# Kernel optimization log

Measured on AMD Instinct MI355X. Metric: run time of the kernel, lower is better.

Reference implementation:

```python
import jax, jax.numpy as jnp
import numpy as np

PHI_C = 0.9
ALPHA = 0.9
EPS = 1e-06
K_MAX = 100


def setup_inputs() -> dict:
    key = jax.random.key(0)
    k1, k2, k3 = jax.random.split(key, 3)
    B, D_IN, D_H, D_OUT = 16384, 1024, 4096, 1024
    x = jax.random.normal(k1, (B, D_IN), dtype=jnp.float32)
    W1 = jax.random.normal(k2, (D_IN, D_H), dtype=jnp.float32) * 0.02
    b1 = jnp.zeros((D_H,), dtype=jnp.float32)
    W2 = jax.random.normal(k3, (D_H, D_OUT), dtype=jnp.float32) * 0.02
    b2 = jnp.zeros((D_OUT,), dtype=jnp.float32)
    return {"x": x, "W1": W1, "b1": b1, "W2": W2, "b2": b2}


def _base_net(x, W1, b1, W2, b2):
    h = jax.nn.relu(x @ W1 + b1)
    return h @ W2 + b2  # [B, D_OUT]


def _fixed_point(out):
    # y_{k+1} = y_k + alpha * phi_c * tanh(out - y_k), with early exit when
    # max|y_{k+1} - y_k| < eps (the converging step IS applied, as in torch).
    y0 = jnp.zeros_like(out)

    def step(carry, _):
        y, done = carry
        y_next = y + ALPHA * PHI_C * jnp.tanh(out - y)
        converged = jnp.max(jnp.abs(y_next - y)) < EPS
        y_new = jnp.where(done, y, y_next)
        return (y_new, done | converged), None

    (y, _), _ = jax.lax.scan(step, (y0, jnp.array(False)), None, length=K_MAX)
    return y


def reference(x, W1, b1, W2, b2):
    out = _base_net(x, W1, b1, W2, b2)
    return _fixed_point(out)
```

## Files before the change

kernel.cpp:

```cpp
#include <hip/hip_runtime.h>
#include <hip/hip_bf16.h>
#include <stdint.h>


#define DEV __device__ __forceinline__

typedef short bf16x8 __attribute__((ext_vector_type(8)));
typedef float f32x4 __attribute__((ext_vector_type(4)));

typedef __attribute__((address_space(1))) const unsigned char* gptr1_t;
typedef __attribute__((address_space(3))) unsigned char* lptr3_t;

DEV void async_copy16(const void* g, void* l) {
  __builtin_amdgcn_global_load_lds((gptr1_t)g, (lptr3_t)l, 16, 0, 0);
}

DEV unsigned short f2bf(float f) {
  union { float f; unsigned u; } v; v.f = f;
  unsigned u = v.u + 0x7FFFu + ((v.u >> 16) & 1u);
  return (unsigned short)(u >> 16);
}

#define BAR()  __builtin_amdgcn_s_barrier()
#define VMW(n) asm volatile("s_waitcnt vmcnt(" #n ")" ::: "memory")


__global__ void cvt_f32_bf16(const float4* __restrict__ in,
                             ushort4* __restrict__ out, int n4) {
  int i = blockIdx.x * blockDim.x + threadIdx.x;
  if (i >= n4) return;
  float4 v = in[i];
  ushort4 o;
  o.x = f2bf(v.x); o.y = f2bf(v.y); o.z = f2bf(v.z); o.w = f2bf(v.w);
  out[i] = o;
}

__global__ void transpose_f32_bf16(const float* __restrict__ in,
                                   unsigned short* __restrict__ out,
                                   int R, int C) {
  __shared__ float tile[32][33];
  int c0 = blockIdx.x * 32, r0 = blockIdx.y * 32;
  int tx = threadIdx.x, ty = threadIdx.y;
#pragma unroll
  for (int i = 0; i < 32; i += 8)
    tile[ty + i][tx] = in[(long)(r0 + ty + i) * C + (c0 + tx)];
  __syncthreads();
#pragma unroll
  for (int i = 0; i < 32; i += 8)
    out[(long)(c0 + ty + i) * R + (r0 + tx)] = f2bf(tile[tx][ty + i]);
}


#define LDA(base, m, ks) \
  (*(const bf16x8*)((base) + abase + (m) * 2048 + (c0 ^ ((ks) << 6))))
#define LDB(base, n, ks) \
  (*(const bf16x8*)((base) + bbase + (n) * 2048 + (c0 ^ ((ks) << 6))))

#define RD_A(dst, base, m0_)                                   \
  _Pragma("unroll") for (int m_ = 0; m_ < 4; ++m_) {           \
    dst[m_][0] = LDA(base, (m0_) + m_, 0);                     \
    dst[m_][1] = LDA(base, (m0_) + m_, 1);                     \
  }
#define RD_B(dst, base, n0_)                                   \
  _Pragma("unroll") for (int n_ = 0; n_ < 2; ++n_) {           \
    dst[n_][0] = LDB(base, (n0_) + n_, 0);                     \
    dst[n_][1] = LDB(base, (n0_) + n_, 1);                     \
  }

#define QUAD(MB, NB, AF, BF)                                                \
  do {                                                                      \
    __builtin_amdgcn_s_setprio(1);                                          \
    _Pragma("unroll") for (int m_ = 0; m_ < 4; ++m_)                        \
    _Pragma("unroll") for (int n_ = 0; n_ < 2; ++n_) {                      \
      acc[(MB) + m_][(NB) + n_] = __builtin_amdgcn_mfma_f32_16x16x32_bf16(  \
          AF[m_][0], BF[n_][0], acc[(MB) + m_][(NB) + n_], 0, 0, 0);        \
      acc[(MB) + m_][(NB) + n_] = __builtin_amdgcn_mfma_f32_16x16x32_bf16(  \
          AF[m_][1], BF[n_][1], acc[(MB) + m_][(NB) + n_], 0, 0, 0);        \
    }                                                                       \
    __builtin_amdgcn_s_setprio(0);                                          \
  } while (0)

#define ST_A_LO(dstw, koff) { async_copy16(gA[0] + (koff), (dstw));          \
                              async_copy16(gA[2] + (koff), (dstw) + 16384); }
#define ST_A_HI(dstw, koff) { async_copy16(gA[1] + (koff), (dstw) + 8192);   \
                              async_copy16(gA[3] + (koff), (dstw) + 24576); }
#define ST_B_LO(dstw, koff) { async_copy16(gB[0] + (koff), (dstw));          \
                              async_copy16(gB[1] + (koff), (dstw) + 8192); }
#define ST_B_HI(dstw, koff) { async_copy16(gB[2] + (koff), (dstw) + 16384);  \
                              async_copy16(gB[3] + (koff), (dstw) + 24576); }


__global__ __launch_bounds__(512, 2)
void gemm_w8p(const unsigned short* __restrict__ A,
              const unsigned short* __restrict__ BT,
              const float* __restrict__ bias,
              unsigned short* __restrict__ O,
              int K, int Ndim) {
  extern __shared__ char lds[];
  const char* aE = lds;
  const char* aO = lds + 32768;
  const char* bE = lds + 65536;
  const char* bO = lds + 98304;

  const int tid = threadIdx.x;
  const int wave = tid >> 6, lane = tid & 63;
  const int wr = wave >> 2, wc = wave & 3;

  char* aEw = (char*)aE + wave * 1024;
  char* aOw = (char*)aO + wave * 1024;
  char* bEw = (char*)bE + wave * 1024;
  char* bOw = (char*)bO + wave * 1024;

  const int xcd = blockIdx.x & 7;
  const int jj = blockIdx.x >> 3;
  const int grp = ((xcd >> 1) << 2) | (jj >> 3);
  const int bn = ((xcd & 1) << 3) | (jj & 7);
  const int n0 = bn << 8;
  const int m0base = grp << 10;

  const int srow = tid >> 3;
  const int sk = ((tid & 7) ^ (srow & 7)) << 3;
  const unsigned short* gA[4];
  const unsigned short* gB[4];
#pragma unroll
  for (int c = 0; c < 4; ++c) {
    gA[c] = A + (size_t)(m0base + c * 64 + srow) * K + sk;
    gB[c] = BT + (size_t)(n0 + c * 64 + srow) * K + sk;
  }

  const int lr = lane & 15, lg = lane >> 4;
  const int c0 = ((lg ^ (lr & 7)) << 4);
  const int abase = (wr * 128 + lr) * 128;
  const int bbase = (wc * 64 + lr) * 128;
  const int ccol = n0 + wc * 64;

  f32x4 acc[8][4] = {};
  bf16x8 af[4][2], b01[2][2], b23[2][2];
  float bv[4];
#pragma unroll
  for (int n = 0; n < 4; ++n) bv[n] = bias[ccol + n * 16 + lr];

#define AOFF(g) ((size_t)((g) >> 4) * ((size_t)K << 8) + (size_t)(((g) & 15) << 6))
#define BOFF(g) ((size_t)(((g) & 15) << 6))

#define PEPI(j_)                                                              \
  { const int crow = m0base + (j_) * 256 + wr * 128;                          \
    _Pragma("unroll") for (int m = 0; m < 8; ++m)                             \
    _Pragma("unroll") for (int jq = 0; jq < 4; ++jq) {                        \
      size_t r = (size_t)(crow + m * 16 + lg * 4 + jq) * Ndim;                \
      _Pragma("unroll") for (int n = 0; n < 4; ++n) {                         \
        float v = acc[m][n][jq] + bv[n];                                      \
        O[r + ccol + n * 16 + lr] = f2bf(fmaxf(v, 0.0f));                     \
      } } }

#define ZEROACC()                                                             \
  _Pragma("unroll") for (int m = 0; m < 8; ++m)                               \
  _Pragma("unroll") for (int n = 0; n < 4; ++n)                               \
    acc[m][n] = (f32x4){0.f, 0.f, 0.f, 0.f};

  ST_B_LO(bEw, 0);        ST_B_HI(bEw, 0);
  ST_A_LO(aEw, 0);        ST_A_HI(aEw, 0);
  ST_B_LO(bOw, BOFF(1));  ST_B_HI(bOw, BOFF(1));
  VMW(4);
  BAR();

  for (int it = 0; it < 31; ++it) {
    const int gE = 2 * it, gO = 2 * it + 1;
    RD_B(b01, bE, 0); RD_A(af, aE, 0); RD_B(b23, bE, 2);
    ST_A_LO(aOw, AOFF(gE + 1)); ST_A_HI(aOw, AOFF(gE + 1));
    QUAD(0, 0, af, b01); QUAD(0, 2, af, b23);
    BAR();
    RD_A(af, aE, 4);
    ST_B_LO(bEw, BOFF(gE + 2)); ST_B_HI(bEw, BOFF(gE + 2));
    QUAD(4, 2, af, b23); QUAD(4, 0, af, b01);
    VMW(4); BAR();
    RD_B(b01, bO, 0); RD_A(af, aO, 0); RD_B(b23, bO, 2);
    ST_A_LO(aEw, AOFF(gO + 1)); ST_A_HI(aEw, AOFF(gO + 1));
    QUAD(0, 0, af, b01); QUAD(0, 2, af, b23);
    BAR();
    RD_A(af, aO, 4);
    ST_B_LO(bOw, BOFF(gO + 2)); ST_B_HI(bOw, BOFF(gO + 2));
    QUAD(4, 2, af, b23); QUAD(4, 0, af, b01);
    VMW(4); BAR();
    if ((it & 7) == 7) {
      PEPI(gO >> 4);
      ZEROACC();
    }
  }
  RD_B(b01, bE, 0); RD_A(af, aE, 0); RD_B(b23, bE, 2);
  ST_A_LO(aOw, AOFF(63)); ST_A_HI(aOw, AOFF(63));
  QUAD(0, 0, af, b01); QUAD(0, 2, af, b23);
  BAR();
  RD_A(af, aE, 4);
  QUAD(4, 2, af, b23); QUAD(4, 0, af, b01);
  VMW(0); BAR();
  RD_B(b01, bO, 0); RD_A(af, aO, 0); RD_B(b23, bO, 2);
  QUAD(0, 0, af, b01); QUAD(0, 2, af, b23);
  BAR();
  RD_A(af, aO, 4);
  QUAD(4, 2, af, b23); QUAD(4, 0, af, b01);
  PEPI(3);
#undef PEPI
#undef ZEROACC
#undef AOFF
#undef BOFF
}


template <bool RELU_BF16>
__global__ __launch_bounds__(512, 2)
void gemm_w8(const unsigned short* __restrict__ A,
             const unsigned short* __restrict__ BT,
             const float* __restrict__ bias,
             void* __restrict__ Cout,
             int M, int N, int K, int nbn_shift) {
  extern __shared__ char lds[];
  const char* aE = lds;
  const char* aO = lds + 32768;
  const char* bE = lds + 65536;
  const char* bO = lds + 98304;

  const int tid = threadIdx.x;
  const int wave = tid >> 6, lane = tid & 63;
  const int wr = wave >> 2, wc = wave & 3;

  char* aEw = (char*)aE + wave * 1024;
  char* aOw = (char*)aO + wave * 1024;
  char* bEw = (char*)bE + wave * 1024;
  char* bOw = (char*)bO + wave * 1024;

  const int nwg = gridDim.x;
  const int wg = blockIdx.x;
  const int swz = (wg & 7) * (nwg >> 3) + (wg >> 3);
  const int bm = swz >> nbn_shift;
  const int bn = swz & ((1 << nbn_shift) - 1);
  const int m0 = bm << 8, n0 = bn << 8;

  const int srow = tid >> 3;
  const int sk = ((tid & 7) ^ (srow & 7)) << 3;
  const unsigned short* gA[4];
  const unsigned short* gB[4];
#pragma unroll
  for (int c = 0; c < 4; ++c) {
    gA[c] = A + (size_t)(m0 + c * 64 + srow) * K + sk;
    gB[c] = BT + (size_t)(n0 + c * 64 + srow) * K + sk;
  }

  const int lr = lane & 15, lg = lane >> 4;
  const int c0 = ((lg ^ (lr & 7)) << 4);
  const int abase = (wr * 128 + lr) * 128;
  const int bbase = (wc * 64 + lr) * 128;

  f32x4 acc[8][4] = {};
  bf16x8 af[4][2], b01[2][2], b23[2][2];

  ST_B_LO(bEw, 0);  ST_B_HI(bEw, 0);
  ST_A_LO(aEw, 0);  ST_A_HI(aEw, 0);
  ST_B_LO(bOw, 64); ST_B_HI(bOw, 64);
  VMW(4);
  BAR();

  const int NT = K >> 6;

  for (int it = 0; it < (NT - 2) / 2; ++it) {
    const int kE = (2 * it) << 6;
    RD_B(b01, bE, 0); RD_A(af, aE, 0); RD_B(b23, bE, 2);
    ST_A_LO(aOw, kE + 64); ST_A_HI(aOw, kE + 64);
    QUAD(0, 0, af, b01); QUAD(0, 2, af, b23);
    BAR();
    RD_A(af, aE, 4);
    ST_B_LO(bEw, kE + 128); ST_B_HI(bEw, kE + 128);
    QUAD(4, 2, af, b23); QUAD(4, 0, af, b01);
    VMW(4); BAR();
    RD_B(b01, bO, 0); RD_A(af, aO, 0); RD_B(b23, bO, 2);
    ST_A_LO(aEw, kE + 128); ST_A_HI(aEw, kE + 128);
    QUAD(0, 0, af, b01); QUAD(0, 2, af, b23);
    BAR();
    RD_A(af, aO, 4);
    ST_B_LO(bOw, kE + 192); ST_B_HI(bOw, kE + 192);
    QUAD(4, 2, af, b23); QUAD(4, 0, af, b01);
    VMW(4); BAR();
  }
  {
    const int kL = (NT - 1) << 6;
    RD_B(b01, bE, 0); RD_A(af, aE, 0); RD_B(b23, bE, 2);
    ST_A_LO(aOw, kL); ST_A_HI(aOw, kL);
    QUAD(0, 0, af, b01); QUAD(0, 2, af, b23);
    BAR();
    RD_A(af, aE, 4);
    QUAD(4, 2, af, b23); QUAD(4, 0, af, b01);
    VMW(0); BAR();
    RD_B(b01, bO, 0); RD_A(af, aO, 0); RD_B(b23, bO, 2);
    QUAD(0, 0, af, b01); QUAD(0, 2, af, b23);
    BAR();
    RD_A(af, aO, 4);
    QUAD(4, 2, af, b23); QUAD(4, 0, af, b01);
  }

  const int ccol = n0 + wc * 64;
  const int crow = m0 + wr * 128;
  float bv[4];
#pragma unroll
  for (int n = 0; n < 4; ++n) bv[n] = bias[ccol + n * 16 + lr];

  if (RELU_BF16) {
    unsigned short* O = (unsigned short*)Cout;
#pragma unroll
    for (int m = 0; m < 8; ++m)
#pragma unroll
      for (int j = 0; j < 4; ++j) {
        size_t r = (size_t)(crow + m * 16 + lg * 4 + j) * N;
#pragma unroll
        for (int n = 0; n < 4; ++n) {
          float v = acc[m][n][j] + bv[n];
          O[r + ccol + n * 16 + lr] = f2bf(fmaxf(v, 0.0f));
        }
      }
  } else {
    float* O = (float*)Cout;
#pragma unroll
    for (int m = 0; m < 8; ++m)
#pragma unroll
      for (int j = 0; j < 4; ++j) {
        size_t r = (size_t)(crow + m * 16 + lg * 4 + j) * N;
#pragma unroll
        for (int n = 0; n < 4; ++n)
          O[r + ccol + n * 16 + lr] = acc[m][n][j] + bv[n];
      }
  }
}


extern "C" void kernel_launch(void* const* d_in, const int* in_sizes, int n_in,
                              void* d_out, int out_size, void* d_ws,
                              size_t ws_size, hipStream_t stream) {
  const float* x  = (const float*)d_in[0];
  const float* W1 = (const float*)d_in[1];
  const float* b1 = (const float*)d_in[2];
  const float* W2 = (const float*)d_in[3];
  const float* b2 = (const float*)d_in[4];
  float* out = (float*)d_out;

  const int B = 16384, DIN = 1024, DH = 4096, DOUT = 1024;

  size_t need = (size_t)B * DIN * 2 + (size_t)DIN * DH * 2 +
                (size_t)DH * DOUT * 2 + (size_t)B * DH * 2;
  if (ws_size < need) return;

  char* ws = (char*)d_ws;
  unsigned short* xb  = (unsigned short*)ws;  ws += (size_t)B * DIN * 2;
  unsigned short* w1t = (unsigned short*)ws;  ws += (size_t)DIN * DH * 2;
  unsigned short* w2t = (unsigned short*)ws;  ws += (size_t)DH * DOUT * 2;
  unsigned short* h   = (unsigned short*)ws;

  hipFuncSetAttribute((const void*)gemm_w8p,
                      hipFuncAttributeMaxDynamicSharedMemorySize, 131072);
  hipFuncSetAttribute((const void*)gemm_w8<false>,
                      hipFuncAttributeMaxDynamicSharedMemorySize, 131072);

  int n4 = B * DIN / 4;
  cvt_f32_bf16<<<n4 / 256, 256, 0, stream>>>((const float4*)x, (ushort4*)xb, n4);
  transpose_f32_bf16<<<dim3(DH / 32, DIN / 32), dim3(32, 8), 0, stream>>>(W1, w1t, DIN, DH);
  transpose_f32_bf16<<<dim3(DOUT / 32, DH / 32), dim3(32, 8), 0, stream>>>(W2, w2t, DH, DOUT);

  gemm_w8p<<<dim3(256), 512, 131072, stream>>>(xb, w1t, b1, h, DIN, DH);
  gemm_w8<false><<<dim3((B / 256) * (DOUT / 256)), 512, 131072, stream>>>(
      h, w2t, b2, out, B, DOUT, DH, 2);
}
```

Before: 264.4 us.

## Triple-buffer A tiles in first GEMM and use nontemporal stores for hidden output

The first GEMM's A operand moves from a two-stage to a three-stage LDS ring, with B staying double-buffered, so loads are issued two k-steps ahead. LDS use rises from 128 KiB to 160 KiB and the wait count is relaxed accordingly. The hidden-activation stores in the epilogue become nontemporal to reduce cache pollution. The larger LDS footprint lowers occupancy from two blocks per CU to one, which could cost more than the deeper prefetch gains.

```diff
diff --git a/kernel.cpp b/kernel.cpp
--- a/kernel.cpp
+++ b/kernel.cpp
@@ -97,19 +97,11 @@
               unsigned short* __restrict__ O,
               int K, int Ndim) {
   extern __shared__ char lds[];
-  const char* aE = lds;
-  const char* aO = lds + 32768;
-  const char* bE = lds + 65536;
-  const char* bO = lds + 98304;
 
   const int tid = threadIdx.x;
   const int wave = tid >> 6, lane = tid & 63;
   const int wr = wave >> 2, wc = wave & 3;
-
-  char* aEw = (char*)aE + wave * 1024;
-  char* aOw = (char*)aO + wave * 1024;
-  char* bEw = (char*)bE + wave * 1024;
-  char* bOw = (char*)bO + wave * 1024;
+  const int woff = wave * 1024;
 
   const int xcd = blockIdx.x & 7;
   const int jj = blockIdx.x >> 3;
@@ -150,7 +142,8 @@
       size_t r = (size_t)(crow + m * 16 + lg * 4 + jq) * Ndim;                \
       _Pragma("unroll") for (int n = 0; n < 4; ++n) {                         \
         float v = acc[m][n][jq] + bv[n];                                      \
-        O[r + ccol + n * 16 + lr] = f2bf(fmaxf(v, 0.0f));                     \
+        __builtin_nontemporal_store(f2bf(fmaxf(v, 0.0f)),                     \
+                                    &O[r + ccol + n * 16 + lr]);              \
       } } }
 
 #define ZEROACC()                                                             \
@@ -158,47 +151,58 @@
   _Pragma("unroll") for (int n = 0; n < 4; ++n)                               \
     acc[m][n] = (f32x4){0.f, 0.f, 0.f, 0.f};
 
-  ST_B_LO(bEw, 0);        ST_B_HI(bEw, 0);
-  ST_A_LO(aEw, 0);        ST_A_HI(aEw, 0);
-  ST_B_LO(bOw, BOFF(1));  ST_B_HI(bOw, BOFF(1));
-  VMW(4);
+  {
+    char* a0w = lds + woff;
+    char* a1w = lds + 32768 + woff;
+    char* b0w = lds + 98304 + woff;
+    char* b1w = lds + 131072 + woff;
+    ST_A_LO(a0w, 0);       ST_A_HI(a0w, 0);
+    ST_B_LO(b0w, 0);       ST_B_HI(b0w, 0);
+    ST_A_LO(a1w, AOFF(1)); ST_A_HI(a1w, AOFF(1));
+    ST_B_LO(b1w, BOFF(1)); ST_B_HI(b1w, BOFF(1));
+  }
+  VMW(8);
   BAR();
 
-  for (int it = 0; it < 31; ++it) {
-    const int gE = 2 * it, gO = 2 * it + 1;
-    RD_B(b01, bE, 0); RD_A(af, aE, 0); RD_B(b23, bE, 2);
-    ST_A_LO(aOw, AOFF(gE + 1)); ST_A_HI(aOw, AOFF(gE + 1));
-    QUAD(0, 0, af, b01); QUAD(0, 2, af, b23);
-    BAR();
-    RD_A(af, aE, 4);
-    ST_B_LO(bEw, BOFF(gE + 2)); ST_B_HI(bEw, BOFF(gE + 2));
-    QUAD(4, 2, af, b23); QUAD(4, 0, af, b01);
-    VMW(4); BAR();
-    RD_B(b01, bO, 0); RD_A(af, aO, 0); RD_B(b23, bO, 2);
-    ST_A_LO(aEw, AOFF(gO + 1)); ST_A_HI(aEw, AOFF(gO + 1));
-    QUAD(0, 0, af, b01); QUAD(0, 2, af, b23);
-    BAR();
-    RD_A(af, aO, 4);
-    ST_B_LO(bOw, BOFF(gO + 2)); ST_B_HI(bOw, BOFF(gO + 2));
-    QUAD(4, 2, af, b23); QUAD(4, 0, af, b01);
-    VMW(4); BAR();
-    if ((it & 7) == 7) {
-      PEPI(gO >> 4);
-      ZEROACC();
-    }
-  }
-  RD_B(b01, bE, 0); RD_A(af, aE, 0); RD_B(b23, bE, 2);
-  ST_A_LO(aOw, AOFF(63)); ST_A_HI(aOw, AOFF(63));
-  QUAD(0, 0, af, b01); QUAD(0, 2, af, b23);
-  BAR();
-  RD_A(af, aE, 4);
-  QUAD(4, 2, af, b23); QUAD(4, 0, af, b01);
-  VMW(0); BAR();
-  RD_B(b01, bO, 0); RD_A(af, aO, 0); RD_B(b23, bO, 2);
-  QUAD(0, 0, af, b01); QUAD(0, 2, af, b23);
-  BAR();
-  RD_A(af, aO, 4);
-  QUAD(4, 2, af, b23); QUAD(4, 0, af, b01);
+  int ia = 0, ia2 = 2, ib = 0;
+  for (int g = 0; g < 62; ++g) {
+    const char* aB = lds + ia * 32768;
+    const char* bB = lds + 98304 + ib * 32768;
+    char* aSw = lds + ia2 * 32768 + woff;
+    char* bSw = lds + 98304 + ib * 32768 + woff;
+    const size_t ka = AOFF(g + 2), kb = BOFF(g + 2);
+    RD_B(b01, bB, 0); RD_A(af, aB, 0); RD_B(b23, bB, 2);
+    ST_A_LO(aSw, ka); ST_A_HI(aSw, ka);
+    QUAD(0, 0, af, b01); QUAD(0, 2, af, b23);
+    BAR();
+    RD_A(af, aB, 4);
+    ST_B_LO(bSw, kb); ST_B_HI(bSw, kb);
+    QUAD(4, 2, af, b23); QUAD(4, 0, af, b01);
+    VMW(8); BAR();
+    if ((g & 15) == 15) { PEPI(g >> 4); ZEROACC(); }
+    ia = (ia == 2) ? 0 : ia + 1;
+    ia2 = (ia2 == 2) ? 0 : ia2 + 1;
+    ib ^= 1;
+  }
+  {
+    const char* aB = lds + 2 * 32768;
+    const char* bB = lds + 98304;
+    RD_B(b01, bB, 0); RD_A(af, aB, 0); RD_B(b23, bB, 2);
+    QUAD(0, 0, af, b01); QUAD(0, 2, af, b23);
+    BAR();
+    RD_A(af, aB, 4);
+    QUAD(4, 2, af, b23); QUAD(4, 0, af, b01);
+    VMW(0); BAR();
+  }
+  {
+    const char* aB = lds;
+    const char* bB = lds + 131072;
+    RD_B(b01, bB, 0); RD_A(af, aB, 0); RD_B(b23, bB, 2);
+    QUAD(0, 0, af, b01); QUAD(0, 2, af, b23);
+    BAR();
+    RD_A(af, aB, 4);
+    QUAD(4, 2, af, b23); QUAD(4, 0, af, b01);
+  }
   PEPI(3);
 #undef PEPI
 #undef ZEROACC
@@ -354,7 +358,7 @@
   unsigned short* h   = (unsigned short*)ws;
 
   hipFuncSetAttribute((const void*)gemm_w8p,
-                      hipFuncAttributeMaxDynamicSharedMemorySize, 131072);
+                      hipFuncAttributeMaxDynamicSharedMemorySize, 163840);
   hipFuncSetAttribute((const void*)gemm_w8<false>,
                       hipFuncAttributeMaxDynamicSharedMemorySize, 131072);
 
@@ -363,7 +367,7 @@
   transpose_f32_bf16<<<dim3(DH / 32, DIN / 32), dim3(32, 8), 0, stream>>>(W1, w1t, DIN, DH);
   transpose_f32_bf16<<<dim3(DOUT / 32, DH / 32), dim3(32, 8), 0, stream>>>(W2, w2t, DH, DOUT);
 
-  gemm_w8p<<<dim3(256), 512, 131072, stream>>>(xb, w1t, b1, h, DIN, DH);
+  gemm_w8p<<<dim3(256), 512, 163840, stream>>>(xb, w1t, b1, h, DIN, DH);
   gemm_w8<false><<<dim3((B / 256) * (DOUT / 256)), 512, 131072, stream>>>(
       h, w2t, b2, out, B, DOUT, DH, 2);
 }
```

Result: no change. 268.1 us (+1.4%).
